# Optimization experiments

Measured on AMD Instinct MI355X. Metric: run time of the kernel, lower is better.

## Reference

```python
import jax, jax.numpy as jnp
import numpy as np

EPS = 1e-5
N_KNN = 16


def _knn_idx(query_feat, ref_feat, k):
    # query_feat: (B, N, C), ref_feat: (B, M, C) -> idx (B, N, k) of smallest sq-dist
    q2 = jnp.sum(query_feat * query_feat, axis=-1, keepdims=True)        # (B,N,1)
    r2 = jnp.sum(ref_feat * ref_feat, axis=-1)[:, None, :]               # (B,1,M)
    d = q2 + r2 - 2.0 * jnp.einsum('bnc,bmc->bnm', query_feat, ref_feat)  # (B,N,M)
    _, idx = jax.lax.top_k(-d, k)
    return idx


def _group(x, idx):
    # x: (B, C, M), idx: (B, N, k) -> (B, C, N, k)
    B, C, M = x.shape
    _, N, k = idx.shape
    flat = jnp.broadcast_to(idx.reshape(B, 1, N * k), (B, C, N * k))
    return jnp.take_along_axis(x, flat, axis=2).reshape(B, C, N, k)


def _bn(x, g, b, m, v):
    # eval-mode BatchNorm2d over channel axis 1 of (B,C,N,k)
    inv = g / jnp.sqrt(v + EPS)
    return x * inv[None, :, None, None] + (b - m * inv)[None, :, None, None]


def setup_inputs() -> dict:
    key = jax.random.key(0)
    ks = jax.random.split(key, 24)
    B, C, N, N2 = 4, 256, 2048, 2048
    ph = 64  # pos_hidden_dim
    ah = 256  # dim * attn_hidden_multiplier = 64*4
    s = lambda fan: 1.0 / np.sqrt(fan)
    inp = {
        'pcd': jax.random.normal(ks[0], (B, 3, N), jnp.float32),
        'feat': jax.random.normal(ks[1], (B, C, N), jnp.float32),
        'pcd_feadb': jax.random.normal(ks[2], (B, 3, N2), jnp.float32),
        'feat_feadb': jax.random.normal(ks[3], (B, C, N2), jnp.float32),
        'pos_w1': jax.random.normal(ks[4], (ph, 3), jnp.float32) * s(3),
        'pos_b1': jax.random.normal(ks[5], (ph,), jnp.float32) * 0.01,
        'pos_g': jax.random.uniform(ks[6], (ph,), jnp.float32, 0.5, 1.5),
        'pos_be': jax.random.normal(ks[7], (ph,), jnp.float32) * 0.01,
        'pos_m': jax.random.normal(ks[8], (ph,), jnp.float32) * 0.1,
        'pos_v': jax.random.uniform(ks[9], (ph,), jnp.float32, 0.5, 1.5),
        'pos_w2': jax.random.normal(ks[10], (C, ph), jnp.float32) * s(ph),
        'pos_b2': jax.random.normal(ks[11], (C,), jnp.float32) * 0.01,
        'attn_w1': jax.random.normal(ks[12], (ah, C), jnp.float32) * s(C),
        'attn_b1': jax.random.normal(ks[13], (ah,), jnp.float32) * 0.01,
        'attn_g': jax.random.uniform(ks[14], (ah,), jnp.float32, 0.5, 1.5),
        'attn_be': jax.random.normal(ks[15], (ah,), jnp.float32) * 0.01,
        'attn_m': jax.random.normal(ks[16], (ah,), jnp.float32) * 0.1,
        'attn_v': jax.random.uniform(ks[17], (ah,), jnp.float32, 0.5, 1.5),
        'attn_w2': jax.random.normal(ks[18], (C, ah), jnp.float32) * s(ah),
        'attn_b2': jax.random.normal(ks[19], (C,), jnp.float32) * 0.01,
    }
    return inp


def reference(pcd, feat, pcd_feadb, feat_feadb,
              pos_w1, pos_b1, pos_g, pos_be, pos_m, pos_v, pos_w2, pos_b2,
              attn_w1, attn_b1, attn_g, attn_be, attn_m, attn_v, attn_w2, attn_b2):
    fusion_pcd = jnp.concatenate([pcd, pcd_feadb], axis=2)    # (B,3,M)
    fusion_feat = jnp.concatenate([feat, feat_feadb], axis=2)  # (B,C,M)
    # KNN in feature space: neighbors of each key point among fusion set
    idx = _knn_idx(jnp.swapaxes(feat, 1, 2), jnp.swapaxes(fusion_feat, 1, 2), N_KNN)  # (B,N,k)
    group_point = _group(fusion_pcd, idx)   # (B,3,N,k)
    group_feat = _group(fusion_feat, idx)   # (B,C,N,k)
    qk_rel = feat[:, :, :, None] - group_feat
    pos_rel = pcd[:, :, :, None] - group_point
    # pos_mlp: conv1x1 -> BN -> relu -> conv1x1
    h = jnp.einsum('oc,bcnk->bonk', pos_w1, pos_rel) + pos_b1[None, :, None, None]
    h = jax.nn.relu(_bn(h, pos_g, pos_be, pos_m, pos_v))
    pos_embedding = jnp.einsum('oc,bcnk->bonk', pos_w2, h) + pos_b2[None, :, None, None]
    # attn_mlp
    a = jnp.einsum('oc,bcnk->bonk', attn_w1, qk_rel + pos_embedding) + attn_b1[None, :, None, None]
    a = jax.nn.relu(_bn(a, attn_g, attn_be, attn_m, attn_v))
    a = jnp.einsum('oc,bcnk->bonk', attn_w2, a) + attn_b2[None, :, None, None]
    sample_weight = jax.nn.softmax(a, axis=-1)  # softmax over the k neighbors
    refined_feat = jnp.sum(sample_weight * (group_feat + pos_embedding), axis=-1)  # (B,C,N)
    return refined_feat
```

## Files before the change

### kernel.cpp

```cpp
#include <hip/hip_runtime.h>
#include <float.h>

#define CDIM 256
#define NPTS 2048
#define MPTS 4096
#define NB   4
#define KNN  16
#define COLS 64
#define NCHUNK 8
#define CSIZE  512
#define NSTEPS 16

typedef _Float16 half8 __attribute__((ext_vector_type(8)));
typedef _Float16 half4 __attribute__((ext_vector_type(4)));
typedef float    f32x4 __attribute__((ext_vector_type(4)));

__device__ __forceinline__ int swzS(int row, int byte) {
    return row * 512 + (byte ^ ((row & 7) << 4));
}
__device__ __forceinline__ int swz128(int row, int byte) {
    return row * 128 + (byte ^ ((row & 7) << 4));
}

__device__ __forceinline__ float sum16(float v) {
    v += __uint_as_float(__builtin_amdgcn_update_dpp(0, __float_as_uint(v), 0x128, 0xF, 0xF, true));
    v += __uint_as_float(__builtin_amdgcn_update_dpp(0, __float_as_uint(v), 0x124, 0xF, 0xF, true));
    v += __uint_as_float(__builtin_amdgcn_update_dpp(0, __float_as_uint(v), 0x122, 0xF, 0xF, true));
    v += __uint_as_float(__builtin_amdgcn_update_dpp(0, __float_as_uint(v), 0x121, 0xF, 0xF, true));
    return v;
}

#define KINS(kk)                                                                \
    {                                                                           \
        unsigned nk_ = (kk);                                                    \
        _Pragma("unroll")                                                       \
        for (int i_ = 0; i_ < 15; i_++) {                                       \
            unsigned lo_ = td[i_] < nk_ ? td[i_] : nk_;                         \
            td[i_] = td[i_ + 1] > lo_ ? td[i_ + 1] : lo_;                       \
        }                                                                       \
        td[15] = td[15] < nk_ ? td[15] : nk_;                                   \
    }

__global__ __launch_bounds__(256) void tposeHL2(const float* __restrict__ feat,
                                                const float* __restrict__ featdb,
                                                _Float16* __restrict__ featH,
                                                _Float16* __restrict__ featL,
                                                float* __restrict__ r2) {
    __shared__ float red[8][33];
    const int b = blockIdx.y;
    const int mt = blockIdx.x;
    const int m = threadIdx.x & 31;
    const int cp = threadIdx.x >> 5;
    const int mg = mt * 32 + m;
    const float* src = (mg < NPTS) ? (feat + (size_t)b * CDIM * NPTS + mg)
                                   : (featdb + (size_t)b * CDIM * NPTS + (mg - NPTS));
    const int c0 = cp * 32;
    float acc = 0.f;
    half8 hh[4], ll[4];
#pragma unroll
    for (int i = 0; i < 32; i++) {
        float v = src[(size_t)(c0 + i) * NPTS];
        acc += v * v;
        _Float16 h = (_Float16)v;
        hh[i >> 3][i & 7] = h;
        ll[i >> 3][i & 7] = (_Float16)(v - (float)h);
    }
    _Float16* dh = featH + ((size_t)b * MPTS + mg) * CDIM + c0;
    _Float16* dl = featL + ((size_t)b * MPTS + mg) * CDIM + c0;
#pragma unroll
    for (int i = 0; i < 4; i++) {
        *(half8*)(dh + i * 8) = hh[i];
        *(half8*)(dl + i * 8) = ll[i];
    }
    red[cp][m] = acc;
    __syncthreads();
    if (threadIdx.x < 32) {
        float s = 0.f;
#pragma unroll
        for (int j = 0; j < 8; j++) s += red[j][threadIdx.x];
        r2[b * MPTS + mt * 32 + threadIdx.x] = s;
    }
}

__global__ __launch_bounds__(256) void wcvt(const float* __restrict__ aw1,
                                            const float* __restrict__ aw2,
                                            const float* __restrict__ pw2,
                                            _Float16* __restrict__ aw1h,
                                            _Float16* __restrict__ aw2h,
                                            _Float16* __restrict__ pw2h) {
    int i = blockIdx.x * 256 + threadIdx.x;
    if (i < 65536) { aw1h[i] = (_Float16)aw1[i]; aw2h[i] = (_Float16)aw2[i]; }
    if (i < 16384) { pw2h[i] = (_Float16)pw2[i]; }
}

__global__ __launch_bounds__(256) void score_knn(const _Float16* __restrict__ featH,
                                                 const _Float16* __restrict__ featL,
                                                 const float* __restrict__ r2g,
                                                 unsigned* __restrict__ partial) {
    __shared__ __align__(16) char sbuf[65536];
    __shared__ float sr2[CSIZE];

    const int tid = threadIdx.x;
    const int lane = tid & 63, wave = tid >> 6;
    const int l15 = lane & 15, l4 = lane >> 4;
    const int chunk = blockIdx.x, qt = blockIdx.y, b = blockIdx.z;
    const int nq = qt * 64 + wave * 16 + l15;
    const int m0 = chunk * CSIZE;

    for (int i = tid; i < CSIZE; i += 256) sr2[i] = r2g[b * MPTS + m0 + i];

    half8 qh[8], ql[8];
    {
        const _Float16* qb = featH + ((size_t)b * MPTS + nq) * CDIM + l4 * 8;
        const _Float16* qL = featL + ((size_t)b * MPTS + nq) * CDIM + l4 * 8;
#pragma unroll
        for (int ks = 0; ks < 8; ks++) {
            qh[ks] = *(const half8*)(qb + ks * 32);
            ql[ks] = *(const half8*)(qL + ks * 32);
        }
    }

    int adr[8];
#pragma unroll
    for (int ks = 0; ks < 8; ks++)
        adr[ks] = (ks * 4 + l4) * 512 + ((l15 * 16) ^ ((ks & 7) << 4));

    int wadr[4];
#pragma unroll
    for (int j = 0; j < 4; j++)
        wadr[j] = ((tid & 7) * 4 + j) * 512 + (((tid >> 3) * 16) ^ ((tid & 7) << 4));
    const char* gH = (const char*)(featH + ((size_t)b * MPTS + m0 + (tid >> 3)) * CDIM) +
                     (tid & 7) * 64;
    const char* gL = (const char*)(featL + ((size_t)b * MPTS + m0 + (tid >> 3)) * CDIM) +
                     (tid & 7) * 64;

    unsigned td[16];
#pragma unroll
    for (int i = 0; i < 16; i++) td[i] = 0xFFFFFFFFu;
    unsigned bk0 = 0, bk1 = 0, bk2 = 0, bk3 = 0, bk4 = 0, bk5 = 0, bk6 = 0, bk7 = 0;
    int bc = 0;

    half8 pH[4], pL[4];
#pragma unroll
    for (int j = 0; j < 4; j++) {
        pH[j] = *(const half8*)(gH + j * 16);
        pL[j] = *(const half8*)(gL + j * 16);
    }
    gH += 32 * CDIM * 2;
    gL += 32 * CDIM * 2;

    for (int s = 0; s < NSTEPS; ++s) {
        char* buf = sbuf + (s & 1) * 32768;
#pragma unroll
        for (int j = 0; j < 4; j++) {
            *(half8*)(buf + wadr[j])         = pH[j];
            *(half8*)(buf + 16384 + wadr[j]) = pL[j];
        }
        __syncthreads();

        if (s < NSTEPS - 1) {
#pragma unroll
            for (int j = 0; j < 4; j++) {
                pH[j] = *(const half8*)(gH + j * 16);
                pL[j] = *(const half8*)(gL + j * 16);
            }
            gH += 32 * CDIM * 2;
            gL += 32 * CDIM * 2;
        }

        unsigned kk[8];
#pragma unroll
        for (int sub = 0; sub < 2; ++sub) {
            f32x4 a0 = {0.f, 0.f, 0.f, 0.f};
            f32x4 a1 = {0.f, 0.f, 0.f, 0.f};
            f32x4 a2 = {0.f, 0.f, 0.f, 0.f};
#pragma unroll
            for (int ks = 0; ks < 8; ks++) {
                half8 ah = *(const half8*)(buf + adr[ks] + sub * 256);
                half8 al = *(const half8*)(buf + 16384 + adr[ks] + sub * 256);
                a0 = __builtin_amdgcn_mfma_f32_16x16x32_f16(ah, qh[ks], a0, 0, 0, 0);
                a1 = __builtin_amdgcn_mfma_f32_16x16x32_f16(ah, ql[ks], a1, 0, 0, 0);
                a2 = __builtin_amdgcn_mfma_f32_16x16x32_f16(al, qh[ks], a2, 0, 0, 0);
            }
            float4 s4 = *(const float4*)(sr2 + s * 32 + sub * 16 + 4 * l4);
            const float sv[4] = {s4.x, s4.y, s4.z, s4.w};
            const int mloc0 = s * 32 + sub * 16 + 4 * l4;
#pragma unroll
            for (int r = 0; r < 4; r++) {
                float d = fmaxf(sv[r] - 2.f * (a0[r] + a1[r] + a2[r]), 0.f);
                unsigned dq = (unsigned)(d * 4096.f);
                dq = dq > 0x7FFFF0u ? 0x7FFFF0u : dq;
                kk[sub * 4 + r] = (dq << 9) | (unsigned)(mloc0 + r);
            }
        }
#pragma unroll
        for (int j = 0; j < 8; j++) {
            unsigned key = kk[j];
            if (key < td[0]) {
                bk7 = bk6; bk6 = bk5; bk5 = bk4; bk4 = bk3;
                bk3 = bk2; bk2 = bk1; bk1 = bk0; bk0 = key; bc++;
            }
        }
        if (__any(bc != 0)) {
            if (bc > 0 && bk0 < td[0]) KINS(bk0);
            if (bc > 1 && bk1 < td[0]) KINS(bk1);
            if (bc > 2 && bk2 < td[0]) KINS(bk2);
            if (bc > 3 && bk3 < td[0]) KINS(bk3);
            if (bc > 4 && bk4 < td[0]) KINS(bk4);
            if (bc > 5 && bk5 < td[0]) KINS(bk5);
            if (bc > 6 && bk6 < td[0]) KINS(bk6);
            if (bc > 7 && bk7 < td[0]) KINS(bk7);
            bc = 0;
        }
    }

#pragma unroll
    for (int j = 1; j < 4; j++) {
#pragma unroll
        for (int e = 0; e < 16; e++) {
            unsigned kv = __shfl_down(td[e], j * 16);
            if (l4 == 0 && kv < td[0]) KINS(kv);
        }
    }
    if (l4 == 0) {
        const size_t qrow = (size_t)b * NPTS + qt * 64 + wave * 16 + l15;
#pragma unroll
        for (int e = 0; e < 16; e++)
            partial[(size_t)(chunk * 16 + e) * (NB * NPTS) + qrow] = td[e];
    }
}

__global__ __launch_bounds__(256) void merge16(const unsigned* __restrict__ partial,
                                               int* __restrict__ idxout) {
    const int row = blockIdx.x * 256 + threadIdx.x;
    unsigned long long td[16];
#pragma unroll
    for (int i = 0; i < 16; i++) td[i] = 0x8000000000ull + (unsigned long long)i;
    unsigned long long curmax = 0x800000000Full;
    for (int e = 0; e < NCHUNK * 16; e++) {
        unsigned k = partial[(size_t)e * (NB * NPTS) + row];
        unsigned long long k64 =
            (((unsigned long long)(k >> 9)) << 12) |
            (unsigned long long)((unsigned)((e >> 4) << 9) | (k & 0x1FFu));
        if (k64 < curmax) {
#pragma unroll
            for (int i_ = 0; i_ < 16; i_++) td[i_] = (td[i_] == curmax) ? k64 : td[i_];
            unsigned long long nm_ = td[0];
#pragma unroll
            for (int i_ = 1; i_ < 16; i_++) nm_ = td[i_] > nm_ ? td[i_] : nm_;
            curmax = nm_;
        }
    }
#pragma unroll
    for (int e = 0; e < 16; e++) idxout[row * 16 + e] = (int)(td[e] & 0xFFFull);
}

__global__ __launch_bounds__(512, 4) void fused_mlp4(
    const float* __restrict__ pcd, const float* __restrict__ pcddb,
    const _Float16* __restrict__ featH, const int* __restrict__ knn,
    const float* __restrict__ pw1, const float* __restrict__ pb1,
    const float* __restrict__ pg, const float* __restrict__ pbe,
    const float* __restrict__ pm, const float* __restrict__ pv,
    const _Float16* __restrict__ pw2h, const float* __restrict__ pb2,
    const _Float16* __restrict__ aw1h, const float* __restrict__ ab1,
    const float* __restrict__ ag, const float* __restrict__ abe,
    const float* __restrict__ am, const float* __restrict__ av,
    const _Float16* __restrict__ aw2h,
    float* __restrict__ out) {
    __shared__ __align__(16) _Float16 xbuf[COLS * 256];
    __shared__ __align__(16) _Float16 pebuf[COLS * 256];
    __shared__ __align__(16) _Float16 hbuf[COLS * 64];
    __shared__ __align__(16) float pr[3][COLS];
    __shared__ int sidx[COLS];
    __shared__ __align__(16) float ainv[256], ash2[256], pinv[64], psh[64];

    const int tid = threadIdx.x;
    const int lane = tid & 63, wave = tid >> 6;
    const int l15 = lane & 15, l4 = lane >> 4;
    const int blk = blockIdx.x;
    const int b = blk >> 9;
    const int n0 = (blk & 511) * 4;
    const int R0 = wave * 32;

    if (tid < COLS) {
        sidx[tid] = knn[(size_t)(b * NPTS + n0 + (tid >> 4)) * KNN + (tid & 15)];
    } else if (tid < COLS + 256) {
        int c = tid - COLS;
        float inv = ag[c] / sqrtf(av[c] + 1e-5f);
        ainv[c] = inv;
        ash2[c] = abe[c] - am[c] * inv + ab1[c] * inv;
    } else if (tid < COLS + 256 + 64) {
        int o = tid - COLS - 256;
        float inv = pg[o] / sqrtf(pv[o] + 1e-5f);
        pinv[o] = inv;
        psh[o] = pbe[o] - pm[o] * inv;
    }
    half8 wp[2][2];
#pragma unroll
    for (int rt = 0; rt < 2; rt++)
#pragma unroll
        for (int ks = 0; ks < 2; ks++)
            wp[rt][ks] = *(const half8*)(pw2h + (size_t)(R0 + rt * 16 + l15) * 64 +
                                         ks * 32 + l4 * 8);
    __syncthreads();

    if (tid < 3 * COLS) {
        int c = tid >> 6, col = tid & 63;
        int m = sidx[col];
        const float* pc = pcd + ((size_t)b * 3 + c) * NPTS;
        const float* px = pcddb + ((size_t)b * 3 + c) * NPTS;
        float gp = (m < NPTS) ? pc[m] : px[m - NPTS];
        pr[c][col] = pc[n0 + (col >> 4)] - gp;
    }
    const int colx = tid & 63;
    const int c0x = (tid >> 6) * 32;
    half8 fmv[4], fnv[4];
    {
        const _Float16* fmp = featH + ((size_t)b * MPTS + sidx[colx]) * CDIM + c0x;
        const _Float16* fnp = featH + ((size_t)b * MPTS + n0 + (colx >> 4)) * CDIM + c0x;
#pragma unroll
        for (int j = 0; j < 4; j++) {
            fmv[j] = *(const half8*)(fmp + j * 8);
            fnv[j] = *(const half8*)(fnp + j * 8);
        }
    }
    __syncthreads();

    {
        int col = tid >> 3, o0 = (tid & 7) * 8;
        float x0 = pr[0][col], x1 = pr[1][col], x2 = pr[2][col];
        half8 hv;
#pragma unroll
        for (int i = 0; i < 8; i++) {
            int o = o0 + i;
            float v = pw1[o * 3] * x0 + pw1[o * 3 + 1] * x1 + pw1[o * 3 + 2] * x2 + pb1[o];
            v = fmaxf(v * pinv[o] + psh[o], 0.f);
            hv[i] = (_Float16)v;
        }
        *(half8*)((char*)hbuf + swz128(col, o0 * 2)) = hv;
    }
    __syncthreads();

    f32x4 acc[2][4];
#pragma unroll
    for (int rt = 0; rt < 2; rt++)
#pragma unroll
        for (int ct = 0; ct < 4; ct++) acc[rt][ct] = (f32x4){0.f, 0.f, 0.f, 0.f};
#pragma unroll
    for (int ks = 0; ks < 2; ks++) {
        int k0 = ks * 32 + l4 * 8;
#pragma unroll
        for (int ct = 0; ct < 4; ct++) {
            half8 bb = *(const half8*)((char*)hbuf + swz128(ct * 16 + l15, k0 * 2));
            acc[0][ct] = __builtin_amdgcn_mfma_f32_16x16x32_f16(wp[0][ks], bb, acc[0][ct], 0, 0, 0);
            acc[1][ct] = __builtin_amdgcn_mfma_f32_16x16x32_f16(wp[1][ks], bb, acc[1][ct], 0, 0, 0);
        }
    }
#pragma unroll
    for (int rt = 0; rt < 2; rt++) {
        int cb = R0 + rt * 16 + 4 * l4;
        float4 pb = *(const float4*)(pb2 + cb);
        float pbv[4] = {pb.x, pb.y, pb.z, pb.w};
#pragma unroll
        for (int ct = 0; ct < 4; ct++) {
            int col = ct * 16 + l15;
            half4 p4;
#pragma unroll
            for (int r = 0; r < 4; r++) p4[r] = (_Float16)(acc[rt][ct][r] + pbv[r]);
            *(half4*)((char*)pebuf + swzS(col, cb * 2)) = p4;
        }
    }
    __syncthreads();

#pragma unroll
    for (int j = 0; j < 4; j++) {
        int c = c0x + j * 8;
        half8 vp = *(const half8*)((char*)pebuf + swzS(colx, c * 2));
        half8 xv = fnv[j] - fmv[j] + vp;
        *(half8*)((char*)xbuf + swzS(colx, c * 2)) = xv;
    }
    half8 wa[2][8];
#pragma unroll
    for (int ks = 0; ks < 8; ks++) {
        wa[0][ks] = *(const half8*)(aw1h + (size_t)(R0 + l15) * 256 + ks * 32 + l4 * 8);
        wa[1][ks] = *(const half8*)(aw1h + (size_t)(R0 + 16 + l15) * 256 + ks * 32 + l4 * 8);
    }
    __syncthreads();

#pragma unroll
    for (int rt = 0; rt < 2; rt++)
#pragma unroll
        for (int ct = 0; ct < 4; ct++) acc[rt][ct] = (f32x4){0.f, 0.f, 0.f, 0.f};
#pragma unroll
    for (int ks = 0; ks < 8; ks++) {
        int k0 = ks * 32 + l4 * 8;
#pragma unroll
        for (int ct = 0; ct < 4; ct++) {
            half8 bb = *(const half8*)((char*)xbuf + swzS(ct * 16 + l15, k0 * 2));
            acc[0][ct] = __builtin_amdgcn_mfma_f32_16x16x32_f16(wa[0][ks], bb, acc[0][ct], 0, 0, 0);
            acc[1][ct] = __builtin_amdgcn_mfma_f32_16x16x32_f16(wa[1][ks], bb, acc[1][ct], 0, 0, 0);
        }
    }
    __syncthreads();

#pragma unroll
    for (int rt = 0; rt < 2; rt++) {
        int cb = R0 + rt * 16 + 4 * l4;
        float4 iv = *(const float4*)(&ainv[cb]);
        float4 sh = *(const float4*)(&ash2[cb]);
        float ivv[4] = {iv.x, iv.y, iv.z, iv.w};
        float shv[4] = {sh.x, sh.y, sh.z, sh.w};
#pragma unroll
        for (int ct = 0; ct < 4; ct++) {
            int col = ct * 16 + l15;
            half4 h4;
#pragma unroll
            for (int r = 0; r < 4; r++)
                h4[r] = (_Float16)fmaxf(acc[rt][ct][r] * ivv[r] + shv[r], 0.f);
            *(half4*)((char*)xbuf + swzS(col, cb * 2)) = h4;
        }
    }
#pragma unroll
    for (int ks = 0; ks < 8; ks++) {
        wa[0][ks] = *(const half8*)(aw2h + (size_t)(R0 + l15) * 256 + ks * 32 + l4 * 8);
        wa[1][ks] = *(const half8*)(aw2h + (size_t)(R0 + 16 + l15) * 256 + ks * 32 + l4 * 8);
    }
    __syncthreads();

#pragma unroll
    for (int rt = 0; rt < 2; rt++)
#pragma unroll
        for (int ct = 0; ct < 4; ct++) acc[rt][ct] = (f32x4){0.f, 0.f, 0.f, 0.f};
#pragma unroll
    for (int ks = 0; ks < 8; ks++) {
        int k0 = ks * 32 + l4 * 8;
#pragma unroll
        for (int ct = 0; ct < 4; ct++) {
            half8 bb = *(const half8*)((char*)xbuf + swzS(ct * 16 + l15, k0 * 2));
            acc[0][ct] = __builtin_amdgcn_mfma_f32_16x16x32_f16(wa[0][ks], bb, acc[0][ct], 0, 0, 0);
            acc[1][ct] = __builtin_amdgcn_mfma_f32_16x16x32_f16(wa[1][ks], bb, acc[1][ct], 0, 0, 0);
        }
    }

    half4 gfa[2][4], pea[2][4];
#pragma unroll
    for (int rt = 0; rt < 2; rt++) {
        int cb = R0 + rt * 16 + 4 * l4;
#pragma unroll
        for (int ct = 0; ct < 4; ct++) {
            int col = ct * 16 + l15;
            gfa[rt][ct] = *(const half4*)(featH + ((size_t)b * MPTS + sidx[col]) * CDIM + cb);
            pea[rt][ct] = *(const half4*)((char*)pebuf + swzS(col, cb * 2));
        }
    }
#pragma unroll
    for (int rt = 0; rt < 2; rt++) {
        int cb = R0 + rt * 16 + 4 * l4;
#pragma unroll
        for (int ct = 0; ct < 4; ct++) {
            float oo[4], ss[4];
#pragma unroll
            for (int r = 0; r < 4; r++) {
                float v = acc[rt][ct][r];
                v = fminf(fmaxf(v, -60.f), 60.f);
                float e = __expf(v);
                float sv = (float)gfa[rt][ct][r] + (float)pea[rt][ct][r];
                ss[r] = sum16(e);
                oo[r] = sum16(e * sv);
            }
            if (l15 < 4) {
                float o = l15 == 0 ? oo[0] : l15 == 1 ? oo[1] : l15 == 2 ? oo[2] : oo[3];
                float s = l15 == 0 ? ss[0] : l15 == 1 ? ss[1] : l15 == 2 ? ss[2] : ss[3];
                out[((size_t)b * CDIM + cb + l15) * NPTS + n0 + ct] =
                    o * __builtin_amdgcn_rcpf(s);
            }
        }
    }
}

extern "C" void kernel_launch(void* const* d_in, const int* in_sizes, int n_in,
                              void* d_out, int out_size, void* d_ws, size_t ws_size,
                              hipStream_t stream) {
    const float* pcd    = (const float*)d_in[0];
    const float* feat   = (const float*)d_in[1];
    const float* pcddb  = (const float*)d_in[2];
    const float* featdb = (const float*)d_in[3];
    const float* pw1 = (const float*)d_in[4];
    const float* pb1 = (const float*)d_in[5];
    const float* pg  = (const float*)d_in[6];
    const float* pbe = (const float*)d_in[7];
    const float* pm  = (const float*)d_in[8];
    const float* pv  = (const float*)d_in[9];
    const float* pw2 = (const float*)d_in[10];
    const float* pb2 = (const float*)d_in[11];
    const float* aw1 = (const float*)d_in[12];
    const float* ab1 = (const float*)d_in[13];
    const float* ag  = (const float*)d_in[14];
    const float* abe = (const float*)d_in[15];
    const float* am  = (const float*)d_in[16];
    const float* av  = (const float*)d_in[17];
    const float* aw2 = (const float*)d_in[18];
    float* out = (float*)d_out;

    char* ws = (char*)d_ws;
    _Float16* featH   = (_Float16*)(ws);
    _Float16* featL   = (_Float16*)(ws + 8388608);
    float*    ws_r2   = (float*)(ws + 16777216);
    unsigned* partial = (unsigned*)(ws + 16842752);
    int*      ws_idx  = (int*)(ws + 21037056);
    _Float16* aw1h    = (_Float16*)(ws + 21561344);
    _Float16* aw2h    = (_Float16*)(ws + 21692416);
    _Float16* pw2h    = (_Float16*)(ws + 21823488);

    wcvt<<<256, 256, 0, stream>>>(aw1, aw2, pw2, aw1h, aw2h, pw2h);
    tposeHL2<<<dim3(MPTS / 32, NB), 256, 0, stream>>>(feat, featdb, featH, featL, ws_r2);
    score_knn<<<dim3(NCHUNK, NPTS / 64, NB), 256, 0, stream>>>(featH, featL, ws_r2, partial);
    merge16<<<NB * NPTS / 256, 256, 0, stream>>>(partial, ws_idx);
    fused_mlp4<<<NB * (NPTS / 4), 512, 0, stream>>>(
        pcd, pcddb, featH, ws_idx,
        pw1, pb1, pg, pbe, pm, pv, pw2h, pb2,
        aw1h, ab1, ag, abe, am, av, aw2h, out);
}
```

Measured before the change: 302.6 us.

## Replace branchy top-k insertion with branch-free bitonic merge networks

Each step's 8 candidate keys now go through a sorting network, are merged into the descending 16-entry top-k list with a bitonic min-merge, and the list is re-sorted with a fixed 32-compare-exchange network. This replaces the data-dependent, divergent insertion path (candidate buffering, __any vote, serial 16-wide inserts). The final cross-lane reduction uses a butterfly xor-shuffle with bitonic merges instead of serial shfl_down insertions. Every step now pays a constant compare-exchange cost even when no candidate qualifies, which may cost more than the old early-out when insertions are rare.

```diff
diff --git a/kernel.cpp b/kernel.cpp
--- a/kernel.cpp
+++ b/kernel.cpp
@@ -30,16 +30,19 @@
     return v;
 }
 
-#define KINS(kk)                                                                \
-    {                                                                           \
-        unsigned nk_ = (kk);                                                    \
-        _Pragma("unroll")                                                       \
-        for (int i_ = 0; i_ < 15; i_++) {                                       \
-            unsigned lo_ = td[i_] < nk_ ? td[i_] : nk_;                         \
-            td[i_] = td[i_ + 1] > lo_ ? td[i_ + 1] : lo_;                       \
-        }                                                                       \
-        td[15] = td[15] < nk_ ? td[15] : nk_;                                   \
-    }
+#define CEA(x, y)                                                               \
+    { unsigned lo_ = kk[x] < kk[y] ? kk[x] : kk[y];                             \
+      unsigned hi_ = kk[x] < kk[y] ? kk[y] : kk[x];                             \
+      kk[x] = lo_; kk[y] = hi_; }
+#define CED(x, y)                                                               \
+    { unsigned hi_ = td[x] > td[y] ? td[x] : td[y];                             \
+      unsigned lo_ = td[x] > td[y] ? td[y] : td[x];                             \
+      td[x] = hi_; td[y] = lo_; }
+#define RESORT16                                                                \
+    CED(0,8) CED(1,9) CED(2,10) CED(3,11) CED(4,12) CED(5,13) CED(6,14) CED(7,15) \
+    CED(0,4) CED(1,5) CED(2,6) CED(3,7) CED(8,12) CED(9,13) CED(10,14) CED(11,15) \
+    CED(0,2) CED(1,3) CED(4,6) CED(5,7) CED(8,10) CED(9,11) CED(12,14) CED(13,15) \
+    CED(0,1) CED(2,3) CED(4,5) CED(6,7) CED(8,9) CED(10,11) CED(12,13) CED(14,15)
 
 __global__ __launch_bounds__(256) void tposeHL2(const float* __restrict__ feat,
                                                 const float* __restrict__ featdb,
@@ -137,8 +140,6 @@
     unsigned td[16];
 #pragma unroll
     for (int i = 0; i < 16; i++) td[i] = 0xFFFFFFFFu;
-    unsigned bk0 = 0, bk1 = 0, bk2 = 0, bk3 = 0, bk4 = 0, bk5 = 0, bk6 = 0, bk7 = 0;
-    int bc = 0;
 
     half8 pH[4], pL[4];
 #pragma unroll
@@ -193,34 +194,30 @@
                 kk[sub * 4 + r] = (dq << 9) | (unsigned)(mloc0 + r);
             }
         }
-#pragma unroll
-        for (int j = 0; j < 8; j++) {
-            unsigned key = kk[j];
-            if (key < td[0]) {
-                bk7 = bk6; bk6 = bk5; bk5 = bk4; bk4 = bk3;
-                bk3 = bk2; bk2 = bk1; bk1 = bk0; bk0 = key; bc++;
-            }
-        }
-        if (__any(bc != 0)) {
-            if (bc > 0 && bk0 < td[0]) KINS(bk0);
-            if (bc > 1 && bk1 < td[0]) KINS(bk1);
-            if (bc > 2 && bk2 < td[0]) KINS(bk2);
-            if (bc > 3 && bk3 < td[0]) KINS(bk3);
-            if (bc > 4 && bk4 < td[0]) KINS(bk4);
-            if (bc > 5 && bk5 < td[0]) KINS(bk5);
-            if (bc > 6 && bk6 < td[0]) KINS(bk6);
-            if (bc > 7 && bk7 < td[0]) KINS(bk7);
-            bc = 0;
-        }
-    }
-
-#pragma unroll
-    for (int j = 1; j < 4; j++) {
+        CEA(0,1) CEA(2,3) CEA(4,5) CEA(6,7)
+        CEA(0,2) CEA(1,3) CEA(4,6) CEA(5,7)
+        CEA(1,2) CEA(5,6) CEA(0,4) CEA(3,7)
+        CEA(1,5) CEA(2,6)
+        CEA(1,4) CEA(3,6)
+        CEA(2,4) CEA(3,5)
+        CEA(3,4)
+#pragma unroll
+        for (int i = 0; i < 8; i++) td[i] = td[i] < kk[i] ? td[i] : kk[i];
+        RESORT16
+    }
+
+#pragma unroll
+    for (int rr = 0; rr < 2; rr++) {
+        const int dx = 16 << rr;
+        unsigned ot[16];
+#pragma unroll
+        for (int e = 0; e < 16; e++) ot[e] = __shfl_xor(td[e], dx);
 #pragma unroll
         for (int e = 0; e < 16; e++) {
-            unsigned kv = __shfl_down(td[e], j * 16);
-            if (l4 == 0 && kv < td[0]) KINS(kv);
-        }
+            unsigned o = ot[15 - e];
+            td[e] = td[e] < o ? td[e] : o;
+        }
+        RESORT16
     }
     if (l4 == 0) {
         const size_t qrow = (size_t)b * NPTS + qt * 64 + wave * 16 + l15;
```

Result: faster. 278.1 us (-8.1%).
